# Optimization experiments

Measured on AMD Instinct MI355X. Metric: run time of the kernel, lower is better.

The kernel has to match this reference:

```python
import jax, jax.numpy as jnp
import numpy as np

N, K, F_IN, F_OUT, P = 50000, 32, 64, 64, 3


def setup_inputs() -> dict:
    key = jax.random.key(0)
    k1, k2, k3, k4, k5 = jax.random.split(key, 5)
    h = jax.random.normal(k1, (N, F_IN), dtype=jnp.float32)
    pos = jax.random.normal(k2, (N, P), dtype=jnp.float32)
    neighbor_idx = jax.random.randint(k3, (N, K), 0, N, dtype=jnp.int32)
    weight = jax.random.normal(k4, (K * F_IN, F_OUT), dtype=jnp.float32) * 0.02
    bias_p = jax.random.normal(k5, (1, F_OUT), dtype=jnp.float32) * 0.02
    return {"h": h, "pos": pos, "neighbor_idx": neighbor_idx,
            "weight": weight, "bias_p": bias_p}


def reference(h, pos, neighbor_idx, weight, bias_p):
    n, k = neighbor_idx.shape
    msgs = h[neighbor_idx]                      # [N, K, F_IN] gather
    diff = pos[:, None, :] - pos[neighbor_idx]  # [N, K, P]
    sq = jnp.sum(diff * diff, axis=2, keepdims=True)  # [N, K, 1]
    # torch: dist[dist==0] = 0.5 ; safe-sqrt avoids NaN grads at 0
    dist = jnp.where(sq == 0.0, 0.5, jnp.sqrt(jnp.where(sq == 0.0, 1.0, sq)))
    wow = (msgs / dist).reshape(n, k * h.shape[1])  # [N, K*F_IN]
    h1 = wow @ weight + bias_p                   # [N, F_OUT]
    return jax.nn.leaky_relu(h1, negative_slope=0.01)
```

## Files before the change

### kernel.cpp

```cpp
#include <hip/hip_runtime.h>


#define N_NODES 50000
#define KN      32
#define FIN     64
#define FOUT    64
#define MTILE   64

typedef __attribute__((ext_vector_type(4))) float    f32x4;
typedef __attribute__((ext_vector_type(8))) _Float16 f16x8;
typedef __attribute__((ext_vector_type(4))) _Float16 f16x4;

__global__ void k_prep(const float* __restrict__ w, _Float16* __restrict__ wf,
                       const float* __restrict__ h, _Float16* __restrict__ hb) {
    __shared__ float s_w[32 * 64];
    const int tid = threadIdx.x;
    if (blockIdx.x < 64) {
        const int kk = blockIdx.x;
        for (int p = tid; p < 32 * 64; p += 256)
            s_w[p] = w[kk * 32 * 64 + p];
        __syncthreads();
        const int t = tid >> 6, lane = tid & 63;
        const int lm = lane & 15, q = lane >> 4;
        f16x8 o;
        #pragma unroll
        for (int i = 0; i < 8; ++i)
            o[i] = (_Float16)s_w[(q * 8 + i) * 64 + t * 16 + lm];
        *(f16x8*)(wf + kk * 2048 + t * 512 + lane * 8) = o;
    } else {
        const int i = (blockIdx.x - 64) * 256 + tid;
        float4 v = ((const float4*)h)[i];
        f16x4 o = { (_Float16)v.x, (_Float16)v.y, (_Float16)v.z, (_Float16)v.w };
        ((f16x4*)hb)[i] = o;
    }
}

__global__ __launch_bounds__(512, 6) void k_main(
        const _Float16* __restrict__ hf,
        const float*    __restrict__ pos,
        const int*      __restrict__ nidx,
        const _Float16* __restrict__ wf,
        const float*    __restrict__ bias,
        float*          __restrict__ out)
{
    __shared__ int2  s_e[KN * MTILE];
    __shared__ float s_red[2 * 64 * 68];

    const int tid = threadIdx.x;
    const int m0  = blockIdx.x * MTILE;

    for (int p = tid; p < MTILE * KN; p += 512) {
        int m = p & 63, k = p >> 6;
        int node = m0 + m;
        int idx = 0; float scl = 0.f;
        if (node < N_NODES) {
            idx = nidx[node * KN + k];
            float dx = pos[node * 3 + 0] - pos[idx * 3 + 0];
            float dy = pos[node * 3 + 1] - pos[idx * 3 + 1];
            float dz = pos[node * 3 + 2] - pos[idx * 3 + 2];
            float sq = dx * dx + dy * dy + dz * dz;
            scl = (sq == 0.f) ? 2.0f : rsqrtf(sq);
        }
        s_e[k * MTILE + m] = make_int2(idx, __float_as_int(scl));
    }
    __syncthreads();

    const int lane = tid & 63, wv = tid >> 6;
    const int lm = lane & 15, q = lane >> 4;
    const int mg = wv & 1;
    const int kg = wv >> 1;

    const _Float16* pb = wf + lane * 8;
    const int ebase = (kg * 8) * MTILE + mg * 32 + lm;

    f32x4 acc[2][4] = {};

    int2 e0 = s_e[ebase], e1 = s_e[ebase + 16];
    const _Float16* pa0 = hf + e0.x * FIN + q * 8;
    const _Float16* pa1 = hf + e1.x * FIN + q * 8;
    f16x8 A00 = *(const f16x8*)pa0, A01 = *(const f16x8*)(pa0 + 32);
    f16x8 A10 = *(const f16x8*)pa1, A11 = *(const f16x8*)(pa1 + 32);
    _Float16 s0 = (_Float16)__int_as_float(e0.y);
    _Float16 s1 = (_Float16)__int_as_float(e1.y);

    #pragma unroll
    for (int knl = 0; knl < 8; ++knl) {
        f16x8 N00, N01, N10, N11;
        _Float16 ns0, ns1;
        if (knl < 7) {
            int eb = ebase + (knl + 1) * MTILE;
            int2 f0 = s_e[eb], f1 = s_e[eb + 16];
            const _Float16* q0 = hf + f0.x * FIN + q * 8;
            const _Float16* q1 = hf + f1.x * FIN + q * 8;
            N00 = *(const f16x8*)q0; N01 = *(const f16x8*)(q0 + 32);
            N10 = *(const f16x8*)q1; N11 = *(const f16x8*)(q1 + 32);
            ns0 = (_Float16)__int_as_float(f0.y);
            ns1 = (_Float16)__int_as_float(f1.y);
        }

        const _Float16* pbb = pb + ((kg * 8 + knl) * 2) * 2048;
        {
            f16x8 a0 = A00 * s0, a1 = A10 * s1;
            f16x8 b0 = *(const f16x8*)(pbb);
            f16x8 b1 = *(const f16x8*)(pbb + 512);
            f16x8 b2 = *(const f16x8*)(pbb + 1024);
            f16x8 b3 = *(const f16x8*)(pbb + 1536);
            acc[0][0] = __builtin_amdgcn_mfma_f32_16x16x32_f16(a0, b0, acc[0][0], 0, 0, 0);
            acc[0][1] = __builtin_amdgcn_mfma_f32_16x16x32_f16(a0, b1, acc[0][1], 0, 0, 0);
            acc[0][2] = __builtin_amdgcn_mfma_f32_16x16x32_f16(a0, b2, acc[0][2], 0, 0, 0);
            acc[0][3] = __builtin_amdgcn_mfma_f32_16x16x32_f16(a0, b3, acc[0][3], 0, 0, 0);
            acc[1][0] = __builtin_amdgcn_mfma_f32_16x16x32_f16(a1, b0, acc[1][0], 0, 0, 0);
            acc[1][1] = __builtin_amdgcn_mfma_f32_16x16x32_f16(a1, b1, acc[1][1], 0, 0, 0);
            acc[1][2] = __builtin_amdgcn_mfma_f32_16x16x32_f16(a1, b2, acc[1][2], 0, 0, 0);
            acc[1][3] = __builtin_amdgcn_mfma_f32_16x16x32_f16(a1, b3, acc[1][3], 0, 0, 0);
        }
        {
            f16x8 a0 = A01 * s0, a1 = A11 * s1;
            f16x8 b0 = *(const f16x8*)(pbb + 2048);
            f16x8 b1 = *(const f16x8*)(pbb + 2560);
            f16x8 b2 = *(const f16x8*)(pbb + 3072);
            f16x8 b3 = *(const f16x8*)(pbb + 3584);
            acc[0][0] = __builtin_amdgcn_mfma_f32_16x16x32_f16(a0, b0, acc[0][0], 0, 0, 0);
            acc[0][1] = __builtin_amdgcn_mfma_f32_16x16x32_f16(a0, b1, acc[0][1], 0, 0, 0);
            acc[0][2] = __builtin_amdgcn_mfma_f32_16x16x32_f16(a0, b2, acc[0][2], 0, 0, 0);
            acc[0][3] = __builtin_amdgcn_mfma_f32_16x16x32_f16(a0, b3, acc[0][3], 0, 0, 0);
            acc[1][0] = __builtin_amdgcn_mfma_f32_16x16x32_f16(a1, b0, acc[1][0], 0, 0, 0);
            acc[1][1] = __builtin_amdgcn_mfma_f32_16x16x32_f16(a1, b1, acc[1][1], 0, 0, 0);
            acc[1][2] = __builtin_amdgcn_mfma_f32_16x16x32_f16(a1, b2, acc[1][2], 0, 0, 0);
            acc[1][3] = __builtin_amdgcn_mfma_f32_16x16x32_f16(a1, b3, acc[1][3], 0, 0, 0);
        }
        if (knl < 7) {
            A00 = N00; A01 = N01; A10 = N10; A11 = N11;
            s0 = ns0; s1 = ns1;
        }
    }

    float* reg = s_red + (kg & 1) * (64 * 68);
    if (kg < 2) {
        #pragma unroll
        for (int mt = 0; mt < 2; ++mt)
            #pragma unroll
            for (int t = 0; t < 4; ++t)
                #pragma unroll
                for (int r = 0; r < 4; ++r)
                    reg[(mg * 32 + mt * 16 + q * 4 + r) * 68 + t * 16 + lm] = acc[mt][t][r];
    }
    __syncthreads();
    if (kg >= 2) {
        #pragma unroll
        for (int mt = 0; mt < 2; ++mt)
            #pragma unroll
            for (int t = 0; t < 4; ++t)
                #pragma unroll
                for (int r = 0; r < 4; ++r)
                    reg[(mg * 32 + mt * 16 + q * 4 + r) * 68 + t * 16 + lm] += acc[mt][t][r];
    }
    __syncthreads();

    const int row = tid >> 3, c0 = (tid & 7) * 8;
    const int node = m0 + row;
    if (node < N_NODES) {
        #pragma unroll
        for (int i = 0; i < 2; ++i) {
            int c = c0 + i * 4;
            f32x4 v0 = *(const f32x4*)(s_red + row * 68 + c);
            f32x4 v1 = *(const f32x4*)(s_red + 64 * 68 + row * 68 + c);
            f32x4 bb = *(const f32x4*)(bias + c);
            f32x4 o = v0 + v1 + bb;
            #pragma unroll
            for (int j = 0; j < 4; ++j) o[j] = o[j] > 0.f ? o[j] : 0.01f * o[j];
            *(f32x4*)(out + node * FOUT + c) = o;
        }
    }
}

extern "C" void kernel_launch(void* const* d_in, const int* in_sizes, int n_in,
                              void* d_out, int out_size, void* d_ws, size_t ws_size,
                              hipStream_t stream) {
    const float* h    = (const float*)d_in[0];
    const float* pos  = (const float*)d_in[1];
    const int*   nidx = (const int*)d_in[2];
    const float* w    = (const float*)d_in[3];
    const float* bias = (const float*)d_in[4];
    float* out = (float*)d_out;

    _Float16* wf = (_Float16*)d_ws;
    _Float16* hb = (_Float16*)((char*)d_ws + 262144);

    k_prep<<<64 + (N_NODES * FIN / 4) / 256, 256, 0, stream>>>(w, wf, h, hb);
    k_main<<<(N_NODES + MTILE - 1) / MTILE, 512, 0, stream>>>(hb, pos, nidx, wf, bias, out);
}
```

Before: 136.1 us.

## Give each wave all 64 rows over 4 neighbors to reuse weight fragments

Work is repartitioned so each of the 8 waves covers all 64 node rows (4 M-tiles) over 4 neighbor slots, instead of 32 rows over 8 neighbor slots. Each weight fragment loaded from global/L2 now feeds 4 M-tiles instead of 2, halving weight load traffic per MFMA. The cost is doubled accumulator and prefetch register state, with launch bounds relaxed from 6 to 2 blocks per CU. The cross-wave reduction also grows from 2 to 4 serialized LDS phases with extra barriers, so lower occupancy may hurt hiding of the gather latency.

```diff
diff --git a/kernel.cpp b/kernel.cpp
--- a/kernel.cpp
+++ b/kernel.cpp
@@ -35,7 +35,7 @@
     }
 }
 
-__global__ __launch_bounds__(512, 6) void k_main(
+__global__ __launch_bounds__(512, 2) void k_main(
         const _Float16* __restrict__ hf,
         const float*    __restrict__ pos,
         const int*      __restrict__ nidx,
@@ -65,95 +65,107 @@
     }
     __syncthreads();
 
-    const int lane = tid & 63, wv = tid >> 6;
+    const int lane = tid & 63, kg = tid >> 6;
     const int lm = lane & 15, q = lane >> 4;
-    const int mg = wv & 1;
-    const int kg = wv >> 1;
 
     const _Float16* pb = wf + lane * 8;
-    const int ebase = (kg * 8) * MTILE + mg * 32 + lm;
-
-    f32x4 acc[2][4] = {};
-
-    int2 e0 = s_e[ebase], e1 = s_e[ebase + 16];
-    const _Float16* pa0 = hf + e0.x * FIN + q * 8;
-    const _Float16* pa1 = hf + e1.x * FIN + q * 8;
-    f16x8 A00 = *(const f16x8*)pa0, A01 = *(const f16x8*)(pa0 + 32);
-    f16x8 A10 = *(const f16x8*)pa1, A11 = *(const f16x8*)(pa1 + 32);
-    _Float16 s0 = (_Float16)__int_as_float(e0.y);
-    _Float16 s1 = (_Float16)__int_as_float(e1.y);
+    const int ebase = (kg * 4) * MTILE + lm;
+
+    f32x4 acc[4][4] = {};
+
+    f16x8   A[4][2];
+    _Float16 sc[4];
+    {
+        #pragma unroll
+        for (int mt = 0; mt < 4; ++mt) {
+            int2 e = s_e[ebase + mt * 16];
+            const _Float16* pa = hf + e.x * FIN + q * 8;
+            A[mt][0] = *(const f16x8*)pa;
+            A[mt][1] = *(const f16x8*)(pa + 32);
+            sc[mt] = (_Float16)__int_as_float(e.y);
+        }
+    }
 
     #pragma unroll
-    for (int knl = 0; knl < 8; ++knl) {
-        f16x8 N00, N01, N10, N11;
-        _Float16 ns0, ns1;
-        if (knl < 7) {
-            int eb = ebase + (knl + 1) * MTILE;
-            int2 f0 = s_e[eb], f1 = s_e[eb + 16];
-            const _Float16* q0 = hf + f0.x * FIN + q * 8;
-            const _Float16* q1 = hf + f1.x * FIN + q * 8;
-            N00 = *(const f16x8*)q0; N01 = *(const f16x8*)(q0 + 32);
-            N10 = *(const f16x8*)q1; N11 = *(const f16x8*)(q1 + 32);
-            ns0 = (_Float16)__int_as_float(f0.y);
-            ns1 = (_Float16)__int_as_float(f1.y);
-        }
-
-        const _Float16* pbb = pb + ((kg * 8 + knl) * 2) * 2048;
-        {
-            f16x8 a0 = A00 * s0, a1 = A10 * s1;
+    for (int j = 0; j < 4; ++j) {
+        f16x8   NA[4][2];
+        _Float16 ns[4];
+        if (j < 3) {
+            #pragma unroll
+            for (int mt = 0; mt < 4; ++mt) {
+                int2 e = s_e[ebase + (j + 1) * MTILE + mt * 16];
+                const _Float16* pa = hf + e.x * FIN + q * 8;
+                NA[mt][0] = *(const f16x8*)pa;
+                NA[mt][1] = *(const f16x8*)(pa + 32);
+                ns[mt] = (_Float16)__int_as_float(e.y);
+            }
+        }
+
+        const int kn = kg * 4 + j;
+        #pragma unroll
+        for (int jh = 0; jh < 2; ++jh) {
+            const _Float16* pbb = pb + (kn * 2 + jh) * 2048;
             f16x8 b0 = *(const f16x8*)(pbb);
             f16x8 b1 = *(const f16x8*)(pbb + 512);
             f16x8 b2 = *(const f16x8*)(pbb + 1024);
             f16x8 b3 = *(const f16x8*)(pbb + 1536);
-            acc[0][0] = __builtin_amdgcn_mfma_f32_16x16x32_f16(a0, b0, acc[0][0], 0, 0, 0);
-            acc[0][1] = __builtin_amdgcn_mfma_f32_16x16x32_f16(a0, b1, acc[0][1], 0, 0, 0);
-            acc[0][2] = __builtin_amdgcn_mfma_f32_16x16x32_f16(a0, b2, acc[0][2], 0, 0, 0);
-            acc[0][3] = __builtin_amdgcn_mfma_f32_16x16x32_f16(a0, b3, acc[0][3], 0, 0, 0);
-            acc[1][0] = __builtin_amdgcn_mfma_f32_16x16x32_f16(a1, b0, acc[1][0], 0, 0, 0);
-            acc[1][1] = __builtin_amdgcn_mfma_f32_16x16x32_f16(a1, b1, acc[1][1], 0, 0, 0);
-            acc[1][2] = __builtin_amdgcn_mfma_f32_16x16x32_f16(a1, b2, acc[1][2], 0, 0, 0);
-            acc[1][3] = __builtin_amdgcn_mfma_f32_16x16x32_f16(a1, b3, acc[1][3], 0, 0, 0);
-        }
-        {
-            f16x8 a0 = A01 * s0, a1 = A11 * s1;
-            f16x8 b0 = *(const f16x8*)(pbb + 2048);
-            f16x8 b1 = *(const f16x8*)(pbb + 2560);
-            f16x8 b2 = *(const f16x8*)(pbb + 3072);
-            f16x8 b3 = *(const f16x8*)(pbb + 3584);
-            acc[0][0] = __builtin_amdgcn_mfma_f32_16x16x32_f16(a0, b0, acc[0][0], 0, 0, 0);
-            acc[0][1] = __builtin_amdgcn_mfma_f32_16x16x32_f16(a0, b1, acc[0][1], 0, 0, 0);
-            acc[0][2] = __builtin_amdgcn_mfma_f32_16x16x32_f16(a0, b2, acc[0][2], 0, 0, 0);
-            acc[0][3] = __builtin_amdgcn_mfma_f32_16x16x32_f16(a0, b3, acc[0][3], 0, 0, 0);
-            acc[1][0] = __builtin_amdgcn_mfma_f32_16x16x32_f16(a1, b0, acc[1][0], 0, 0, 0);
-            acc[1][1] = __builtin_amdgcn_mfma_f32_16x16x32_f16(a1, b1, acc[1][1], 0, 0, 0);
-            acc[1][2] = __builtin_amdgcn_mfma_f32_16x16x32_f16(a1, b2, acc[1][2], 0, 0, 0);
-            acc[1][3] = __builtin_amdgcn_mfma_f32_16x16x32_f16(a1, b3, acc[1][3], 0, 0, 0);
-        }
-        if (knl < 7) {
-            A00 = N00; A01 = N01; A10 = N10; A11 = N11;
-            s0 = ns0; s1 = ns1;
+            #pragma unroll
+            for (int mt = 0; mt < 4; ++mt) {
+                f16x8 a = A[mt][jh] * sc[mt];
+                acc[mt][0] = __builtin_amdgcn_mfma_f32_16x16x32_f16(a, b0, acc[mt][0], 0, 0, 0);
+                acc[mt][1] = __builtin_amdgcn_mfma_f32_16x16x32_f16(a, b1, acc[mt][1], 0, 0, 0);
+                acc[mt][2] = __builtin_amdgcn_mfma_f32_16x16x32_f16(a, b2, acc[mt][2], 0, 0, 0);
+                acc[mt][3] = __builtin_amdgcn_mfma_f32_16x16x32_f16(a, b3, acc[mt][3], 0, 0, 0);
+            }
+        }
+
+        if (j < 3) {
+            #pragma unroll
+            for (int mt = 0; mt < 4; ++mt) {
+                A[mt][0] = NA[mt][0]; A[mt][1] = NA[mt][1]; sc[mt] = ns[mt];
+            }
         }
     }
 
     float* reg = s_red + (kg & 1) * (64 * 68);
     if (kg < 2) {
         #pragma unroll
-        for (int mt = 0; mt < 2; ++mt)
-            #pragma unroll
-            for (int t = 0; t < 4; ++t)
-                #pragma unroll
-                for (int r = 0; r < 4; ++r)
-                    reg[(mg * 32 + mt * 16 + q * 4 + r) * 68 + t * 16 + lm] = acc[mt][t][r];
-    }
-    __syncthreads();
-    if (kg >= 2) {
-        #pragma unroll
-        for (int mt = 0; mt < 2; ++mt)
-            #pragma unroll
-            for (int t = 0; t < 4; ++t)
-                #pragma unroll
-                for (int r = 0; r < 4; ++r)
-                    reg[(mg * 32 + mt * 16 + q * 4 + r) * 68 + t * 16 + lm] += acc[mt][t][r];
+        for (int mt = 0; mt < 4; ++mt)
+            #pragma unroll
+            for (int t = 0; t < 4; ++t)
+                #pragma unroll
+                for (int r = 0; r < 4; ++r)
+                    reg[(mt * 16 + q * 4 + r) * 68 + t * 16 + lm] = acc[mt][t][r];
+    }
+    __syncthreads();
+    if (kg >= 2 && kg < 4) {
+        #pragma unroll
+        for (int mt = 0; mt < 4; ++mt)
+            #pragma unroll
+            for (int t = 0; t < 4; ++t)
+                #pragma unroll
+                for (int r = 0; r < 4; ++r)
+                    reg[(mt * 16 + q * 4 + r) * 68 + t * 16 + lm] += acc[mt][t][r];
+    }
+    __syncthreads();
+    if (kg >= 4 && kg < 6) {
+        #pragma unroll
+        for (int mt = 0; mt < 4; ++mt)
+            #pragma unroll
+            for (int t = 0; t < 4; ++t)
+                #pragma unroll
+                for (int r = 0; r < 4; ++r)
+                    reg[(mt * 16 + q * 4 + r) * 68 + t * 16 + lm] += acc[mt][t][r];
+    }
+    __syncthreads();
+    if (kg >= 6) {
+        #pragma unroll
+        for (int mt = 0; mt < 4; ++mt)
+            #pragma unroll
+            for (int t = 0; t < 4; ++t)
+                #pragma unroll
+                for (int r = 0; r < 4; ++r)
+                    reg[(mt * 16 + q * 4 + r) * 68 + t * 16 + lm] += acc[mt][t][r];
     }
     __syncthreads();
 
```

After: 145.1 us. 1.07x slower.
